# Kernel tuning notes

Hardware: AMD Instinct MI355X
Metric: run time of the kernel (lower is better)

## Reference

```python
import jax, jax.numpy as jnp
import numpy as np

BATCH = 50          # hardcoded in the layer: self.batch_size = 50
MAX_ATOMS = 21000   # static pad cap; >> N/BATCH + 6*std, so it always covers the dynamic max


def setup_inputs() -> dict:
    key = jax.random.key(0)
    k1, k2 = jax.random.split(key)
    N, D = 1_000_000, 128
    atom_features = jax.random.normal(k1, (N, D), dtype=jnp.float32)
    atom_partition_indices = jnp.sort(
        jax.random.randint(k2, (N,), 0, BATCH, dtype=jnp.int64))
    return {"atom_features": atom_features,
            "atom_partition_indices": atom_partition_indices}


def reference(atom_features, atom_partition_indices):
    N, D = atom_features.shape
    # Per-partition counts and start offsets (indices are sorted, as produced
    # by tf.dynamic_partition's stable ordering for sorted ids).
    counts = jnp.bincount(atom_partition_indices, length=BATCH)          # [B]
    starts = jnp.cumsum(counts) - counts                                  # [B]
    # Position of each atom within its partition.
    pos = jnp.arange(N) - starts[atom_partition_indices]                  # [N]
    # Fused scatter-to-padded-tensor: one pass instead of 50 partition/pad ops.
    padded = jnp.zeros((BATCH, MAX_ATOMS, D), atom_features.dtype)
    padded = padded.at[atom_partition_indices, pos].set(atom_features)    # [B, MAX, D]
    # Keep only nonempty examples (sum over atoms+features != 0), like
    # tf.where + tf.gather. Static-size nonzero keeps this jit-compatible;
    # with these inputs every partition is nonempty so this is exact.
    mask = jnp.sum(padded, axis=(1, 2)) != 0                              # [B]
    keep = jnp.nonzero(mask, size=BATCH, fill_value=0)[0]
    return padded[keep]
```

## Files before the change

kernel.cpp:

```cpp
#include <hip/hip_runtime.h>

#define BATCH 50
#define MAX_ATOMS 21000
#define DIM 128
#define ROW4 (DIM / 4)

__global__ void compute_starts_kernel(const int* __restrict__ idx32, int N,
                                      int* __restrict__ starts) {
    __shared__ int s_is64;
    if (threadIdx.x == 0) {
        int flag = 0;
        int base = N / 2;
        int lim = N - 1;
        for (int k = 0; k < 256 && (base + k + 1) <= lim; ++k) {
            if (idx32[base + k] > idx32[base + k + 1]) { flag = 1; break; }
        }
        s_is64 = flag;
    }
    __syncthreads();
    const int stride = s_is64 ? 2 : 1;

    int b = threadIdx.x;
    if (b <= BATCH) {
        int lo = 0, hi = N;
        while (lo < hi) {
            int mid = (lo + hi) >> 1;
            int v = idx32[(long)mid * stride];
            if (v < b) lo = mid + 1; else hi = mid;
        }
        starts[b] = lo;
    }
}

__global__ __launch_bounds__(256) void gather_pad_kernel(
        const float4* __restrict__ feat,
        const int* __restrict__ starts,
        float4* __restrict__ out) {
    unsigned int gid = blockIdx.x * 256u + threadIdx.x;
    const unsigned int total4 = (unsigned int)BATCH * MAX_ATOMS * ROW4;
    if (gid >= total4) return;

    unsigned int q   = gid & (ROW4 - 1);
    unsigned int row = gid >> 5;
    unsigned int b   = row / MAX_ATOMS;
    unsigned int p   = row - b * MAX_ATOMS;

    int s   = starts[b];
    int cnt = starts[b + 1] - s;

    float4 v = make_float4(0.f, 0.f, 0.f, 0.f);
    if ((int)p < cnt) {
        v = feat[(long)(s + (int)p) * ROW4 + q];
    }
    out[gid] = v;
}

extern "C" void kernel_launch(void* const* d_in, const int* in_sizes, int n_in,
                              void* d_out, int out_size, void* d_ws, size_t ws_size,
                              hipStream_t stream) {
    const float* feat = (const float*)d_in[0];
    const int*   idx  = (const int*)d_in[1];
    int N = in_sizes[1];

    int* starts = (int*)d_ws;

    compute_starts_kernel<<<1, 64, 0, stream>>>(idx, N, starts);

    const long total4 = (long)BATCH * MAX_ATOMS * ROW4;
    const int  block  = 256;
    const int  grid   = (int)((total4 + block - 1) / block);
    gather_pad_kernel<<<grid, block, 0, stream>>>(
        (const float4*)feat, starts, (float4*)d_out);
}
```

Before: 200.3 us.

## Speed up start search via sampled bisection; use nontemporal 4-per-thread copy

The starts kernel now detects index width with a wavefront ballot instead of a serial scan. It samples 1024 index values into shared memory and runs a coarse bisection there before a short fine search in global memory, which cuts the serial dependent global loads. The gather kernel caches the starts in shared memory, processes four float4 per thread, and uses nontemporal loads and stores so the large streaming output does not pollute the cache. The output write of about 538MB dominates, so any gains depend on how the nontemporal stores behave.

```diff
diff --git a/kernel.cpp b/kernel.cpp
--- a/kernel.cpp
+++ b/kernel.cpp
@@ -4,55 +4,82 @@
 #define MAX_ATOMS 21000
 #define DIM 128
 #define ROW4 (DIM / 4)
+#define TOTAL4 (BATCH * MAX_ATOMS * ROW4)
+#define SAMPLES 1024
 
-__global__ void compute_starts_kernel(const int* __restrict__ idx32, int N,
-                                      int* __restrict__ starts) {
-    __shared__ int s_is64;
-    if (threadIdx.x == 0) {
-        int flag = 0;
+typedef float f4 __attribute__((ext_vector_type(4)));
+
+__global__ __launch_bounds__(1024) void compute_starts_kernel(
+        const int* __restrict__ idx32, int N, int* __restrict__ starts) {
+    __shared__ int s_flag;
+    __shared__ int samp[SAMPLES];
+
+    if (threadIdx.x < 64) {
         int base = N / 2;
-        int lim = N - 1;
-        for (int k = 0; k < 256 && (base + k + 1) <= lim; ++k) {
-            if (idx32[base + k] > idx32[base + k + 1]) { flag = 1; break; }
-        }
-        s_is64 = flag;
+        int a = idx32[base + threadIdx.x];
+        int c = idx32[base + threadIdx.x + 1];
+        unsigned long long m = __ballot(a > c);
+        if (threadIdx.x == 0) s_flag = (m != 0ull) ? 1 : 0;
     }
     __syncthreads();
-    const int stride = s_is64 ? 2 : 1;
+    const int stride = s_flag ? 2 : 1;
+    const int step = (N + SAMPLES - 1) / SAMPLES;
+
+    {
+        int t = threadIdx.x;
+        int i = t * step; if (i > N - 1) i = N - 1;
+        samp[t] = idx32[(long)i * stride];
+    }
+    __syncthreads();
 
     int b = threadIdx.x;
     if (b <= BATCH) {
-        int lo = 0, hi = N;
+        int ulo = 0, uhi = SAMPLES;
+        while (ulo < uhi) {
+            int m = (ulo + uhi) >> 1;
+            if (samp[m] < b) ulo = m + 1; else uhi = m;
+        }
+        int lo, hi;
+        if (ulo == 0) { lo = 0; hi = 1; }
+        else {
+            int j = (ulo - 1) * step; if (j > N - 1) j = N - 1;
+            lo = j + 1;
+            if (ulo == SAMPLES) hi = N;
+            else { int k = ulo * step; if (k > N - 1) k = N - 1; hi = k + 1; }
+        }
         while (lo < hi) {
-            int mid = (lo + hi) >> 1;
-            int v = idx32[(long)mid * stride];
-            if (v < b) lo = mid + 1; else hi = mid;
+            int m = (lo + hi) >> 1;
+            if (idx32[(long)m * stride] < b) lo = m + 1; else hi = m;
         }
         starts[b] = lo;
     }
 }
 
 __global__ __launch_bounds__(256) void gather_pad_kernel(
-        const float4* __restrict__ feat,
+        const f4* __restrict__ feat,
         const int* __restrict__ starts,
-        float4* __restrict__ out) {
-    unsigned int gid = blockIdx.x * 256u + threadIdx.x;
-    const unsigned int total4 = (unsigned int)BATCH * MAX_ATOMS * ROW4;
-    if (gid >= total4) return;
+        f4* __restrict__ out) {
+    __shared__ int s_starts[BATCH + 1];
+    if (threadIdx.x <= BATCH) s_starts[threadIdx.x] = starts[threadIdx.x];
+    __syncthreads();
 
-    unsigned int q   = gid & (ROW4 - 1);
-    unsigned int row = gid >> 5;
-    unsigned int b   = row / MAX_ATOMS;
-    unsigned int p   = row - b * MAX_ATOMS;
-
-    int s   = starts[b];
-    int cnt = starts[b + 1] - s;
-
-    float4 v = make_float4(0.f, 0.f, 0.f, 0.f);
-    if ((int)p < cnt) {
-        v = feat[(long)(s + (int)p) * ROW4 + q];
+    unsigned int base = blockIdx.x * 1024u + threadIdx.x;
+#pragma unroll
+    for (int k = 0; k < 4; ++k) {
+        unsigned int gid = base + (unsigned)k * 256u;
+        if (gid < (unsigned)TOTAL4) {
+            unsigned int q   = gid & (ROW4 - 1);
+            unsigned int row = gid >> 5;
+            unsigned int b   = row / MAX_ATOMS;
+            unsigned int p   = row - b * MAX_ATOMS;
+            int s = s_starts[b];
+            int e = s_starts[b + 1];
+            f4 v = (f4)(0.0f);
+            if ((int)p < e - s)
+                v = __builtin_nontemporal_load(feat + (long)(s + (int)p) * ROW4 + q);
+            __builtin_nontemporal_store(v, out + gid);
+        }
     }
-    out[gid] = v;
 }
 
 extern "C" void kernel_launch(void* const* d_in, const int* in_sizes, int n_in,
@@ -64,11 +91,9 @@
 
     int* starts = (int*)d_ws;
 
-    compute_starts_kernel<<<1, 64, 0, stream>>>(idx, N, starts);
+    compute_starts_kernel<<<1, 1024, 0, stream>>>(idx, N, starts);
 
-    const long total4 = (long)BATCH * MAX_ATOMS * ROW4;
-    const int  block  = 256;
-    const int  grid   = (int)((total4 + block - 1) / block);
-    gather_pad_kernel<<<grid, block, 0, stream>>>(
-        (const float4*)feat, starts, (float4*)d_out);
+    const int grid = (TOTAL4 + 1023) / 1024;
+    gather_pad_kernel<<<grid, 256, 0, stream>>>(
+        (const f4*)feat, starts, (f4*)d_out);
 }
```

After: 182.2 us. -9.0%, faster.
